# Kernel tuning notes

Measured on AMD Instinct MI355X. Metric: run time of the kernel, lower is better.

The kernel has to match this reference:

```python
import jax, jax.numpy as jnp
import numpy as np

N, D, H = 4096, 1024, 2048


def positional_encoding(d_model, n):
    even_i = jnp.arange(0, d_model, 2, dtype=jnp.float32)
    denom = jnp.power(jnp.float32(10000.0), even_i / d_model)
    pos = jnp.arange(n, dtype=jnp.float32)[:, None]            # (N,1)
    even_pe = jnp.sin(pos / denom)                             # (N,D/2)
    odd_pe = jnp.cos(pos / denom)                              # (N,D/2)
    # interleave sin/cos: stack on axis 2 then flatten -> (N, D)
    return jnp.stack([even_pe, odd_pe], axis=2).reshape(n, d_model)


def setup_inputs() -> dict:
    key = jax.random.key(0)
    ks = jax.random.split(key, 5)
    X = jax.random.normal(ks[0], (N, D), dtype=jnp.float32)
    mask = jnp.ones((N,), dtype=jnp.int32)  # unused by the module
    Wv = jax.random.normal(ks[1], (D, D), dtype=jnp.float32) * 0.02
    bv = jnp.zeros((D,), dtype=jnp.float32)
    W1 = jax.random.normal(ks[2], (2 * D, H), dtype=jnp.float32) * 0.02
    b1 = jnp.zeros((H,), dtype=jnp.float32)
    W2 = jax.random.normal(ks[3], (H, N), dtype=jnp.float32) * 0.02
    b2 = jnp.zeros((N,), dtype=jnp.float32)
    return {"X": X, "mask": mask, "Wv": Wv, "bv": bv,
            "W1": W1, "b1": b1, "W2": W2, "b2": b2}


def reference(X, mask, Wv, bv, W1, b1, W2, b2):
    n, d = X.shape
    V = X @ Wv + bv                                            # (N,D)
    PE = positional_encoding(d, n).astype(X.dtype)
    E = PE * X                                                 # (N,D)
    # leave-one-out mean: (global sum - row_i) / (N-1)  [replaces O(N^2) loop]
    loo = (jnp.sum(E, axis=0, keepdims=True) - E) / (n - 1)    # (N,D)
    feat = jnp.concatenate([X, loo], axis=1)                   # (N,2D)
    hidden = jax.nn.relu(feat @ W1 + b1)                       # (N,H)
    att_scores = hidden @ W2 + b2                              # (N,N)
    att_weights = jax.nn.softmax(att_scores, axis=-1)          # (N,N)
    # dropout p=0 (inference) -> identity
    return att_weights @ V                                     # (N,D)
```

## Files before the change

### kernel.cpp

```cpp
#include <hip/hip_runtime.h>
#include <hip/hip_bf16.h>

#define TOK 4096
#define DIM 1024
#define HID 2048
#define LN10K 9.210340371976184f

typedef __bf16 bh;
typedef __bf16 v8bf __attribute__((ext_vector_type(8)));
typedef float v4f __attribute__((ext_vector_type(4)));

typedef const __attribute__((address_space(1))) void* gvp;
typedef __attribute__((address_space(3))) void* svp;

__device__ __forceinline__ void gl_lds16(const bh* g, bh* s) {
  __builtin_amdgcn_global_load_lds((gvp)g, (svp)s, 16, 0, 0);
}

__global__ __launch_bounds__(256) void prep_x_colsum(const float* __restrict__ X,
                                                     bh* __restrict__ featb,
                                                     float* __restrict__ S) {
  int cp = blockIdx.x * 256 + threadIdx.x;
  int c = cp * 2;
  int r0 = blockIdx.y * 16;
  float inv_denom = __expf(-(float)c * (LN10K / (float)DIM));
  float s0 = 0.f, s1 = 0.f;
#pragma unroll 4
  for (int r = r0; r < r0 + 16; ++r) {
    float2 x = *(const float2*)(X + (size_t)r * DIM + c);
    float sn, cs;
    __sincosf((float)r * inv_denom, &sn, &cs);
    s0 += sn * x.x;
    s1 += cs * x.y;
    bh pair[2] = {(bh)x.x, (bh)x.y};
    *(ushort2*)(featb + (size_t)r * (2 * DIM) + c) = *(ushort2*)pair;
  }
  atomicAdd(&S[c], s0);
  atomicAdd(&S[c + 1], s1);
}

__global__ __launch_bounds__(256) void prep_loo(const float* __restrict__ X,
                                                const float* __restrict__ S,
                                                bh* __restrict__ featb) {
  size_t e4 = ((size_t)blockIdx.x * 256 + threadIdx.x) * 4;
  int r = (int)(e4 >> 10);
  int c = (int)(e4 & 1023);
  float4 x = *(const float4*)(X + e4);
  float4 s = *(const float4*)(S + c);
  float id0 = __expf(-(float)c * (LN10K / (float)DIM));
  float id1 = __expf(-(float)(c + 2) * (LN10K / (float)DIM));
  float sn0, cs0, sn1, cs1;
  __sincosf((float)r * id0, &sn0, &cs0);
  __sincosf((float)r * id1, &sn1, &cs1);
  const float inv = 1.0f / (float)(TOK - 1);
  bh outv[4];
  outv[0] = (bh)((s.x - sn0 * x.x) * inv);
  outv[1] = (bh)((s.y - cs0 * x.y) * inv);
  outv[2] = (bh)((s.z - sn1 * x.z) * inv);
  outv[3] = (bh)((s.w - cs1 * x.w) * inv);
  *(ushort4*)(featb + (size_t)r * (2 * DIM) + DIM + c) = *(ushort4*)outv;
}

__global__ __launch_bounds__(256) void transpose_all(const float* __restrict__ Wv,
                                                     const float* __restrict__ W1,
                                                     const float* __restrict__ W2,
                                                     bh* __restrict__ WvT,
                                                     bh* __restrict__ W1T,
                                                     bh* __restrict__ W2T) {
  __shared__ float tile[32][33];
  int bid = blockIdx.x;
  const float* in; bh* out; int Ncol, R, bx, by;
  if (bid < 1024)      { in = Wv; out = WvT; Ncol = DIM; R = DIM;
                         bx = bid & 31; by = bid >> 5; }
  else if (bid < 5120) { int b = bid - 1024; in = W1; out = W1T; Ncol = HID; R = 2 * DIM;
                         bx = b & 63; by = b >> 6; }
  else                 { int b = bid - 5120; in = W2; out = W2T; Ncol = TOK; R = HID;
                         bx = b & 127; by = b >> 7; }
  int nb = bx * 32, rb = by * 32;
  int tx = threadIdx.x, ty = threadIdx.y;
#pragma unroll
  for (int j = 0; j < 32; j += 8)
    tile[ty + j][tx] = in[(size_t)(rb + ty + j) * Ncol + nb + tx];
  __syncthreads();
#pragma unroll
  for (int j = 0; j < 32; j += 8)
    out[(size_t)(nb + ty + j) * R + rb + tx] = (bh)tile[tx][ty + j];
}

template <int BN, bool RELU, bool TROUT, bool EXPS, typename OutT>
__global__ __launch_bounds__(128, 2) void gemm_bt(const bh* __restrict__ A,
                                                  const bh* __restrict__ BT,
                                                  const float* __restrict__ bias,
                                                  OutT* __restrict__ C,
                                                  float* __restrict__ rowsum,
                                                  int K, int lda, int ldbt, int ldc) {
  constexpr int NT = BN / 16;
  __shared__ bh As[128 * 64];
  __shared__ bh Bs[BN * 64];
  const int t = threadIdx.x;
  const int id = blockIdx.x;
  const int bm = (id & 31) * 128, bn = (id >> 5) * BN;

  const int sr = t >> 3;
  const int c8 = ((t & 7) ^ (sr & 7)) * 8;
  const bh* gA = A + (size_t)(bm + sr) * lda + c8;
  const bh* gB = BT + (size_t)(bn + sr) * ldbt + c8;
  bh* sA = As + t * 8;
  bh* sB = Bs + t * 8;

  const int lane = t & 63, w = t >> 6;
  const int lc = lane & 15, q = lane >> 4;

  v4f acc[4][NT] = {};
  for (int k0 = 0; k0 < K; k0 += 64) {
#pragma unroll
    for (int j = 0; j < 8; ++j)
      gl_lds16(gA + k0 + j * 16 * lda, sA + j * 1024);
#pragma unroll
    for (int j = 0; j < NT; ++j)
      gl_lds16(gB + k0 + j * 16 * ldbt, sB + j * 1024);
    __syncthreads();
#pragma unroll
    for (int h = 0; h < 2; ++h) {
      const int off = ((h * 4 + q) ^ (lc & 7)) * 8;
      v8bf af[4], bfr[NT];
#pragma unroll
      for (int mt = 0; mt < 4; ++mt)
        af[mt] = *(const v8bf*)(As + (w * 64 + mt * 16 + lc) * 64 + off);
#pragma unroll
      for (int nt = 0; nt < NT; ++nt)
        bfr[nt] = *(const v8bf*)(Bs + (nt * 16 + lc) * 64 + off);
#pragma unroll
      for (int mt = 0; mt < 4; ++mt)
#pragma unroll
        for (int nt = 0; nt < NT; ++nt)
          acc[mt][nt] = __builtin_amdgcn_mfma_f32_16x16x32_bf16(af[mt], bfr[nt], acc[mt][nt], 0, 0, 0);
    }
    __syncthreads();
  }

  const int r4 = q * 4;
  if (EXPS) {
    float bbv[NT];
#pragma unroll
    for (int nt = 0; nt < NT; ++nt) bbv[nt] = bias ? bias[bn + nt * 16 + lc] : 0.0f;
#pragma unroll
    for (int mt = 0; mt < 4; ++mt) {
#pragma unroll
      for (int r = 0; r < 4; ++r) {
        int row = bm + w * 64 + mt * 16 + r4 + r;
        float rs = 0.0f;
#pragma unroll
        for (int nt = 0; nt < NT; ++nt) {
          float val = __expf(acc[mt][nt][r] + bbv[nt]);
          rs += val;
          C[(size_t)row * ldc + bn + nt * 16 + lc] = (OutT)val;
        }
        rs += __shfl_xor(rs, 1);
        rs += __shfl_xor(rs, 2);
        rs += __shfl_xor(rs, 4);
        rs += __shfl_xor(rs, 8);
        if (lc == 0) atomicAdd(rowsum + row, rs);
      }
    }
  } else {
#pragma unroll
    for (int mt = 0; mt < 4; ++mt) {
      int row0 = bm + w * 64 + mt * 16 + r4;
#pragma unroll
      for (int nt = 0; nt < NT; ++nt) {
        int col = bn + nt * 16 + lc;
        float bb = bias ? bias[col] : 0.0f;
#pragma unroll
        for (int r = 0; r < 4; ++r) {
          float val = acc[mt][nt][r] + bb;
          if (RELU) val = fmaxf(val, 0.0f);
          if (TROUT) C[(size_t)col * ldc + (row0 + r)] = (OutT)val;
          else       C[(size_t)(row0 + r) * ldc + col] = (OutT)val;
        }
      }
    }
  }
}

__global__ __launch_bounds__(256, 4) void gemm4_split(const bh* __restrict__ A,
                                                      const bh* __restrict__ BT,
                                                      float* __restrict__ C0,
                                                      float* __restrict__ C1) {
  __shared__ bh As[128 * 64];
  __shared__ bh Bs[128 * 64];
  const int t = threadIdx.x;
  const int id = blockIdx.x;
  const int bm = (id & 31) * 128, bn = (id >> 5) * 128;
  const int kbeg = blockIdx.y * (TOK / 2);

  const int sr = t >> 3;
  const int c8 = ((t & 7) ^ (sr & 7)) * 8;
  const bh* gA = A + (size_t)(bm + sr) * TOK + kbeg + c8;
  const bh* gB = BT + (size_t)(bn + sr) * TOK + kbeg + c8;
  bh* sA = As + t * 8;
  bh* sB = Bs + t * 8;

  const int lane = t & 63, w = t >> 6;
  const int wm = (w >> 1) * 64, wn = (w & 1) * 64;
  const int lc = lane & 15, q = lane >> 4;

  v4f acc[4][4] = {};
  for (int k0 = 0; k0 < TOK / 2; k0 += 64) {
#pragma unroll
    for (int j = 0; j < 4; ++j) {
      gl_lds16(gA + k0 + (size_t)(j * 32) * TOK, sA + j * 2048);
      gl_lds16(gB + k0 + (size_t)(j * 32) * TOK, sB + j * 2048);
    }
    __syncthreads();
#pragma unroll
    for (int h = 0; h < 2; ++h) {
      const int off = ((h * 4 + q) ^ (lc & 7)) * 8;
      v8bf af[4], bfr[4];
#pragma unroll
      for (int mt = 0; mt < 4; ++mt)
        af[mt] = *(const v8bf*)(As + (wm + mt * 16 + lc) * 64 + off);
#pragma unroll
      for (int nt = 0; nt < 4; ++nt)
        bfr[nt] = *(const v8bf*)(Bs + (wn + nt * 16 + lc) * 64 + off);
#pragma unroll
      for (int mt = 0; mt < 4; ++mt)
#pragma unroll
        for (int nt = 0; nt < 4; ++nt)
          acc[mt][nt] = __builtin_amdgcn_mfma_f32_16x16x32_bf16(af[mt], bfr[nt], acc[mt][nt], 0, 0, 0);
    }
    __syncthreads();
  }

  float* C = blockIdx.y ? C1 : C0;
  const int r4 = q * 4;
#pragma unroll
  for (int mt = 0; mt < 4; ++mt) {
    int row0 = bm + wm + mt * 16 + r4;
#pragma unroll
    for (int nt = 0; nt < 4; ++nt) {
      int col = bn + wn + nt * 16 + lc;
#pragma unroll
      for (int r = 0; r < 4; ++r)
        C[(size_t)(row0 + r) * DIM + col] = acc[mt][nt][r];
    }
  }
}

__global__ __launch_bounds__(256) void finalize(const float* __restrict__ p0,
                                                const float* __restrict__ p1,
                                                const float* __restrict__ rowsum,
                                                float* __restrict__ out) {
  size_t i = ((size_t)blockIdx.x * 256 + threadIdx.x) * 4;
  int row = (int)(i >> 10);
  float inv = 1.0f / rowsum[row];
  float4 a = *(const float4*)(p0 + i);
  float4 b = *(const float4*)(p1 + i);
  float4 o;
  o.x = (a.x + b.x) * inv; o.y = (a.y + b.y) * inv;
  o.z = (a.z + b.z) * inv; o.w = (a.w + b.w) * inv;
  *(float4*)(out + i) = o;
}

extern "C" void kernel_launch(void* const* d_in, const int* in_sizes, int n_in,
                              void* d_out, int out_size, void* d_ws, size_t ws_size,
                              hipStream_t stream) {
  (void)in_sizes; (void)n_in; (void)out_size; (void)ws_size;
  const float* X  = (const float*)d_in[0];
  const float* Wv = (const float*)d_in[2];
  const float* bv = (const float*)d_in[3];
  const float* W1 = (const float*)d_in[4];
  const float* b1 = (const float*)d_in[5];
  const float* W2 = (const float*)d_in[6];
  const float* b2 = (const float*)d_in[7];
  float* out = (float*)d_out;

  char* ws = (char*)d_ws;
  bh* featb = (bh*)(ws);
  bh* WvT   = (bh*)(ws + (16u << 20));
  bh* W1T   = (bh*)(ws + (18u << 20));
  bh* W2T   = (bh*)(ws + (26u << 20));
  bh* Vt    = (bh*)(ws + (42u << 20));
  bh* hid   = (bh*)(ws + (50u << 20));
  bh* scr   = (bh*)(ws + (66u << 20));
  float* S  = (float*)(ws + (98u << 20));
  float* rowsum = (float*)(ws + (98u << 20) + 4096);
  float* part0 = (float*)(ws);
  float* part1 = (float*)(ws + (26u << 20));

  hipError_t e = hipMemsetAsync(S, 0, 4096 + 4096 * sizeof(float), stream);
  (void)e;
  prep_x_colsum<<<dim3(DIM / 512, TOK / 16), 256, 0, stream>>>(X, featb, S);
  prep_loo<<<dim3((TOK * DIM) / 1024), 256, 0, stream>>>(X, S, featb);
  transpose_all<<<dim3(1024 + 4096 + 8192), dim3(32, 8), 0, stream>>>(
      Wv, W1, W2, WvT, W1T, W2T);

  gemm_bt<64, false, true, false, bh><<<dim3(32 * (DIM / 64)), 128, 0, stream>>>(
      featb, WvT, bv, Vt, nullptr, DIM, 2 * DIM, DIM, TOK);
  gemm_bt<128, true, false, false, bh><<<dim3(32 * (HID / 128)), 128, 0, stream>>>(
      featb, W1T, b1, hid, nullptr, 2 * DIM, 2 * DIM, 2 * DIM, HID);
  gemm_bt<128, false, false, true, bh><<<dim3(32 * (TOK / 128)), 128, 0, stream>>>(
      hid, W2T, b2, scr, rowsum, HID, HID, HID, TOK);
  gemm4_split<<<dim3(256, 2), 256, 0, stream>>>(scr, Vt, part0, part1);
  finalize<<<dim3((TOK * DIM) / 1024), 256, 0, stream>>>(part0, part1, rowsum, out);
}
```

Before: 322.2 us.

## Replace scores GEMM with 256x256-tile triple-buffered exp kernel

Adds a dedicated kernel for the hidden@W2 score GEMM that computes 256x256 output tiles with 8 waves of 512 threads. It stages operands into LDS through a three-buffer ring using direct global-to-LDS loads and interleaves staging with MFMA halves. The epilogue applies bias and exp, stores bf16 scores and atomically accumulates row sums. Larger tiles raise data reuse and cut global traffic, at the cost of more registers, only 256 blocks, and more barriers per K step.

```diff
diff --git a/kernel.cpp b/kernel.cpp
--- a/kernel.cpp
+++ b/kernel.cpp
@@ -183,6 +183,119 @@
   }
 }
 
+__global__ __launch_bounds__(512, 2) void gemm_exp256(const bh* __restrict__ A,
+                                                      const bh* __restrict__ BT,
+                                                      const float* __restrict__ bias,
+                                                      bh* __restrict__ C,
+                                                      float* __restrict__ rowsum) {
+  __shared__ bh As[3 * 8192];
+  __shared__ bh Bs[3 * 8192];
+  const int t = threadIdx.x;
+  const int id = blockIdx.x;
+  const int bm = (id & 15) * 256, bn = (id >> 4) * 256;
+  const int lane = t & 63, w = t >> 6;
+  const int wm = (w >> 2) * 128, wn = (w & 3) * 64;
+  const int lc = lane & 15, q = lane >> 4;
+  const int csw = (q ^ ((lc >> 1) & 3)) * 8;
+
+  const int srow = t >> 2;
+  const int sc = (t & 3) ^ ((t >> 3) & 3);
+  const bh* gA = A + (size_t)(bm + srow) * HID + sc * 8;
+  const bh* gB = BT + (size_t)(bn + srow) * HID + sc * 8;
+  bh* sA = As + t * 8;
+  bh* sB = Bs + t * 8;
+
+  auto stage_a = [&](int kt, int buf) {
+    const bh* g = gA + (size_t)kt * 32;
+    bh* s = sA + buf * 8192;
+    gl_lds16(g, s);
+    gl_lds16(g + (size_t)128 * HID, s + 4096);
+  };
+  auto stage_b = [&](int kt, int buf) {
+    const bh* g = gB + (size_t)kt * 32;
+    bh* s = sB + buf * 8192;
+    gl_lds16(g, s);
+    gl_lds16(g + (size_t)128 * HID, s + 4096);
+  };
+
+  v4f acc[8][4] = {};
+
+  stage_a(0, 0); stage_b(0, 0);
+  stage_a(1, 1); stage_b(1, 1);
+  asm volatile("s_waitcnt vmcnt(4)" ::: "memory");
+  __builtin_amdgcn_s_barrier();
+  __builtin_amdgcn_sched_barrier(0);
+
+  int cur = 0, nxt = 2;
+  for (int kt = 0; kt < 64; ++kt) {
+    const bh* ab = As + cur * 8192;
+    const bh* bb = Bs + cur * 8192;
+    v8bf af[4], bf[4];
+#pragma unroll
+    for (int mt = 0; mt < 4; ++mt)
+      af[mt] = *(const v8bf*)(ab + (wm + mt * 16 + lc) * 32 + csw);
+#pragma unroll
+    for (int nt = 0; nt < 4; ++nt)
+      bf[nt] = *(const v8bf*)(bb + (wn + nt * 16 + lc) * 32 + csw);
+    if (kt < 62) stage_a(kt + 2, nxt);
+    __builtin_amdgcn_s_barrier();
+    __builtin_amdgcn_sched_barrier(0);
+    __builtin_amdgcn_s_setprio(1);
+#pragma unroll
+    for (int mt = 0; mt < 4; ++mt)
+#pragma unroll
+      for (int nt = 0; nt < 4; ++nt)
+        acc[mt][nt] = __builtin_amdgcn_mfma_f32_16x16x32_bf16(af[mt], bf[nt], acc[mt][nt], 0, 0, 0);
+    __builtin_amdgcn_s_setprio(0);
+    __builtin_amdgcn_s_barrier();
+    __builtin_amdgcn_sched_barrier(0);
+    v8bf ah[4];
+#pragma unroll
+    for (int mt = 0; mt < 4; ++mt)
+      ah[mt] = *(const v8bf*)(ab + (wm + 64 + mt * 16 + lc) * 32 + csw);
+    if (kt < 62) stage_b(kt + 2, nxt);
+    __builtin_amdgcn_s_barrier();
+    __builtin_amdgcn_sched_barrier(0);
+    __builtin_amdgcn_s_setprio(1);
+#pragma unroll
+    for (int mt = 0; mt < 4; ++mt)
+#pragma unroll
+      for (int nt = 0; nt < 4; ++nt)
+        acc[4 + mt][nt] = __builtin_amdgcn_mfma_f32_16x16x32_bf16(ah[mt], bf[nt], acc[4 + mt][nt], 0, 0, 0);
+    __builtin_amdgcn_s_setprio(0);
+    if (kt < 62)       asm volatile("s_waitcnt vmcnt(4)" ::: "memory");
+    else if (kt == 62) asm volatile("s_waitcnt vmcnt(0)" ::: "memory");
+    __builtin_amdgcn_s_barrier();
+    __builtin_amdgcn_sched_barrier(0);
+    cur = (cur == 2) ? 0 : cur + 1;
+    nxt = (nxt == 2) ? 0 : nxt + 1;
+  }
+
+  const int r4 = q * 4;
+  float bbv[4];
+#pragma unroll
+  for (int nt = 0; nt < 4; ++nt) bbv[nt] = bias[bn + wn + nt * 16 + lc];
+#pragma unroll
+  for (int mt = 0; mt < 8; ++mt) {
+#pragma unroll
+    for (int r = 0; r < 4; ++r) {
+      int row = bm + wm + mt * 16 + r4 + r;
+      float rs = 0.0f;
+#pragma unroll
+      for (int nt = 0; nt < 4; ++nt) {
+        float val = __expf(acc[mt][nt][r] + bbv[nt]);
+        rs += val;
+        C[(size_t)row * TOK + bn + wn + nt * 16 + lc] = (bh)val;
+      }
+      rs += __shfl_xor(rs, 1);
+      rs += __shfl_xor(rs, 2);
+      rs += __shfl_xor(rs, 4);
+      rs += __shfl_xor(rs, 8);
+      if (lc == 0) atomicAdd(rowsum + row, rs);
+    }
+  }
+}
+
 __global__ __launch_bounds__(256, 4) void gemm4_split(const bh* __restrict__ A,
                                                       const bh* __restrict__ BT,
                                                       float* __restrict__ C0,
@@ -299,8 +412,7 @@
       featb, WvT, bv, Vt, nullptr, DIM, 2 * DIM, DIM, TOK);
   gemm_bt<128, true, false, false, bh><<<dim3(32 * (HID / 128)), 128, 0, stream>>>(
       featb, W1T, b1, hid, nullptr, 2 * DIM, 2 * DIM, 2 * DIM, HID);
-  gemm_bt<128, false, false, true, bh><<<dim3(32 * (TOK / 128)), 128, 0, stream>>>(
-      hid, W2T, b2, scr, rowsum, HID, HID, HID, TOK);
+  gemm_exp256<<<dim3(256), 512, 0, stream>>>(hid, W2T, b2, scr, rowsum);
   gemm4_split<<<dim3(256, 2), 256, 0, stream>>>(scr, Vt, part0, part1);
   finalize<<<dim3((TOK * DIM) / 1024), 256, 0, stream>>>(part0, part1, rowsum, out);
 }
```

New measurement: 330.6 us. 1.03x slower.

## Add 256x256 tiled exp GEMM with 4-stage LDS pipeline for attention scores

Applied to the files above, without the earlier changes.

Replaces the generic 128-tile GEMM that computes the exp'd attention scores with a specialised kernel. It uses 512 threads per block, 256x256 output tiles and a 4-slot LDS ring filled by direct global-to-LDS loads. Prefetch runs two tiles ahead with explicit vmcnt waits and raised priority around the MFMA block. The goal is more operand reuse per byte loaded and better overlap of loads with MFMA on the largest GEMM. In exchange it needs more LDS and registers per block, so occupancy is lower, and fewer blocks (256) fill the chip.

```diff
diff --git a/kernel.cpp b/kernel.cpp
--- a/kernel.cpp
+++ b/kernel.cpp
@@ -183,6 +183,110 @@
   }
 }
 
+__global__ __launch_bounds__(512, 2) void gemm_exp256(const bh* __restrict__ A,
+                                                      const bh* __restrict__ BT,
+                                                      const float* __restrict__ bias,
+                                                      bh* __restrict__ C,
+                                                      float* __restrict__ rowsum) {
+  __shared__ bh As[4 * 8192];
+  __shared__ bh Bs[4 * 8192];
+  const int t = threadIdx.x;
+  const int id = blockIdx.x;
+  const int bm = (id & 15) * 256, bn = (id >> 4) * 256;
+  const int lane = t & 63, w = t >> 6;
+  const int wm = (w >> 2) * 128, wn = (w & 3) * 64;
+  const int lc = lane & 15, q = lane >> 4;
+  const int csw = (q ^ ((lc >> 1) & 3)) * 8;
+
+  const int srow = t >> 2;
+  const int sc = (t & 3) ^ ((t >> 3) & 3);
+  const bh* gA = A + (size_t)(bm + srow) * HID + sc * 8;
+  const bh* gB = BT + (size_t)(bn + srow) * HID + sc * 8;
+  bh* sA = As + t * 8;
+  bh* sB = Bs + t * 8;
+
+  v4f acc[8][4] = {};
+
+#define STAGE(kt, slot)                                                        \
+  do {                                                                         \
+    gl_lds16(gA + (kt) * 32, sA + (slot) * 8192);                              \
+    gl_lds16(gA + (kt) * 32 + (size_t)128 * HID, sA + (slot) * 8192 + 4096);   \
+    gl_lds16(gB + (kt) * 32, sB + (slot) * 8192);                              \
+    gl_lds16(gB + (kt) * 32 + (size_t)128 * HID, sB + (slot) * 8192 + 4096);   \
+  } while (0)
+
+#define TILE(kt, slot, STG, WMODE)                                             \
+  do {                                                                         \
+    const bh* ab = As + (slot) * 8192;                                         \
+    const bh* bb = Bs + (slot) * 8192;                                         \
+    v8bf af[4], ah[4], bfr[4];                                                 \
+    _Pragma("unroll") for (int mt = 0; mt < 4; ++mt)                           \
+        af[mt] = *(const v8bf*)(ab + (wm + mt * 16 + lc) * 32 + csw);          \
+    _Pragma("unroll") for (int nt = 0; nt < 4; ++nt)                           \
+        bfr[nt] = *(const v8bf*)(bb + (wn + nt * 16 + lc) * 32 + csw);         \
+    _Pragma("unroll") for (int mt = 0; mt < 4; ++mt)                           \
+        ah[mt] = *(const v8bf*)(ab + (wm + 64 + mt * 16 + lc) * 32 + csw);     \
+    if (STG) STAGE((kt) + 2, ((slot) + 2) & 3);                                \
+    __builtin_amdgcn_s_setprio(1);                                             \
+    _Pragma("unroll") for (int mt = 0; mt < 4; ++mt)                           \
+        _Pragma("unroll") for (int nt = 0; nt < 4; ++nt)                       \
+            acc[mt][nt] = __builtin_amdgcn_mfma_f32_16x16x32_bf16(             \
+                af[mt], bfr[nt], acc[mt][nt], 0, 0, 0);                        \
+    _Pragma("unroll") for (int mt = 0; mt < 4; ++mt)                           \
+        _Pragma("unroll") for (int nt = 0; nt < 4; ++nt)                       \
+            acc[4 + mt][nt] = __builtin_amdgcn_mfma_f32_16x16x32_bf16(         \
+                ah[mt], bfr[nt], acc[4 + mt][nt], 0, 0, 0);                    \
+    __builtin_amdgcn_s_setprio(0);                                             \
+    if ((WMODE) == 1) asm volatile("s_waitcnt vmcnt(4)" ::: "memory");         \
+    if ((WMODE) == 2) asm volatile("s_waitcnt vmcnt(0)" ::: "memory");         \
+    if ((WMODE) != 0) __builtin_amdgcn_s_barrier();                            \
+  } while (0)
+
+  STAGE(0, 0);
+  STAGE(1, 1);
+  asm volatile("s_waitcnt vmcnt(4)" ::: "memory");
+  __builtin_amdgcn_s_barrier();
+
+  for (int ko = 0; ko < 15; ++ko) {
+    const int kb = ko * 4;
+    TILE(kb + 0, 0, true, 1);
+    TILE(kb + 1, 1, true, 1);
+    TILE(kb + 2, 2, true, 1);
+    TILE(kb + 3, 3, true, 1);
+  }
+  TILE(60, 0, true, 1);
+  TILE(61, 1, true, 1);
+  TILE(62, 2, false, 2);
+  TILE(63, 3, false, 0);
+
+#undef TILE
+#undef STAGE
+
+  const int r4 = q * 4;
+  float bbv[4];
+#pragma unroll
+  for (int nt = 0; nt < 4; ++nt) bbv[nt] = bias[bn + wn + nt * 16 + lc];
+#pragma unroll
+  for (int mt = 0; mt < 8; ++mt) {
+#pragma unroll
+    for (int r = 0; r < 4; ++r) {
+      int row = bm + wm + mt * 16 + r4 + r;
+      float rs = 0.0f;
+#pragma unroll
+      for (int nt = 0; nt < 4; ++nt) {
+        float val = __expf(acc[mt][nt][r] + bbv[nt]);
+        rs += val;
+        C[(size_t)row * TOK + bn + wn + nt * 16 + lc] = (bh)val;
+      }
+      rs += __shfl_xor(rs, 1);
+      rs += __shfl_xor(rs, 2);
+      rs += __shfl_xor(rs, 4);
+      rs += __shfl_xor(rs, 8);
+      if (lc == 0) atomicAdd(rowsum + row, rs);
+    }
+  }
+}
+
 __global__ __launch_bounds__(256, 4) void gemm4_split(const bh* __restrict__ A,
                                                       const bh* __restrict__ BT,
                                                       float* __restrict__ C0,
@@ -299,8 +403,7 @@
       featb, WvT, bv, Vt, nullptr, DIM, 2 * DIM, DIM, TOK);
   gemm_bt<128, true, false, false, bh><<<dim3(32 * (HID / 128)), 128, 0, stream>>>(
       featb, W1T, b1, hid, nullptr, 2 * DIM, 2 * DIM, 2 * DIM, HID);
-  gemm_bt<128, false, false, true, bh><<<dim3(32 * (TOK / 128)), 128, 0, stream>>>(
-      hid, W2T, b2, scr, rowsum, HID, HID, HID, TOK);
+  gemm_exp256<<<dim3(256), 512, 0, stream>>>(hid, W2T, b2, scr, rowsum);
   gemm4_split<<<dim3(256, 2), 256, 0, stream>>>(scr, Vt, part0, part1);
   finalize<<<dim3((TOK * DIM) / 1024), 256, 0, stream>>>(part0, part1, rowsum, out);
 }
```

Result: no change. 328.2 us (+1.9%).

## Replace scores GEMM with 256x256-tile pipelined exp kernel

Applied to the files above, without the earlier changes.

Adds a dedicated kernel for the hidden@W2 scores GEMM that uses 256x256 block tiles, 8 waves, and double-buffered direct global-to-LDS loads. The loads for later k-tiles are interleaved between quarter-tile MFMA phases, with barriers and raised wave priority around each phase. The exp epilogue and row-sum atomics are fused in as before. The aim is higher operand reuse and better overlap of memory traffic with MFMA on the largest GEMM. The cost is more LDS and registers per block, and hand-tuned waitcnt counts that must match the issued loads exactly.

```diff
diff --git a/kernel.cpp b/kernel.cpp
--- a/kernel.cpp
+++ b/kernel.cpp
@@ -183,6 +183,151 @@
   }
 }
 
+__global__ __launch_bounds__(512, 2) void gemm_exp256(const bh* __restrict__ A,
+                                                      const bh* __restrict__ BT,
+                                                      const float* __restrict__ bias,
+                                                      bh* __restrict__ C,
+                                                      float* __restrict__ rowsum) {
+  __shared__ bh As[2][16384];
+  __shared__ bh Bs[2][16384];
+  const int t = threadIdx.x;
+  const int id = blockIdx.x;
+  const int bm = (id & 15) * 256, bn = (id >> 4) * 256;
+  const int lane = t & 63, w = t >> 6;
+  const int wm = (w >> 2) * 128, wn = (w & 3) * 64;
+  const int lc = lane & 15, q = lane >> 4;
+  const int e0 = q ^ (lc & 7);
+
+  const int srow = t >> 3;
+  const int schunk = (t & 7) ^ (srow & 7);
+  const bh* gA = A + (size_t)(bm + srow) * HID + schunk * 8;
+  const bh* gB = BT + (size_t)(bn + srow) * HID + schunk * 8;
+  bh* sA = &As[0][0] + t * 8;
+  bh* sB = &Bs[0][0] + t * 8;
+
+  v4f acc[8][4] = {};
+
+#define STG_A(kt, c, buf) \
+  gl_lds16(gA + (size_t)(kt) * 64 + (size_t)((c) * 64) * HID, sA + (buf) * 16384 + (c) * 4096)
+#define STG_B(kt, c, buf) \
+  gl_lds16(gB + (size_t)(kt) * 64 + (size_t)((c) * 64) * HID, sB + (buf) * 16384 + (c) * 4096)
+
+#define TILE64(kt, buf, STG1, STG23, WM)                                        \
+  do {                                                                          \
+    const bh* ab = &As[buf][0];                                                 \
+    const bh* bb = &Bs[buf][0];                                                 \
+    v8bf alo[4][2], ahi[4][2], blo[2][2], bhi2[2][2];                           \
+                                                             \
+    _Pragma("unroll") for (int mt = 0; mt < 4; ++mt)                            \
+      _Pragma("unroll") for (int kk = 0; kk < 2; ++kk)                          \
+        alo[mt][kk] = *(const v8bf*)(ab + (wm + mt * 16 + lc) * 64 +            \
+                                     ((e0 ^ (kk << 2)) << 3));                  \
+    _Pragma("unroll") for (int nt = 0; nt < 2; ++nt)                            \
+      _Pragma("unroll") for (int kk = 0; kk < 2; ++kk)                          \
+        blo[nt][kk] = *(const v8bf*)(bb + (wn + nt * 16 + lc) * 64 +            \
+                                     ((e0 ^ (kk << 2)) << 3));                  \
+    if (STG1) { STG_B((kt) + 1, 2, (buf) ^ 1); STG_B((kt) + 1, 3, (buf) ^ 1); } \
+    __builtin_amdgcn_s_barrier();                                               \
+    asm volatile("s_waitcnt lgkmcnt(0)" ::: "memory");                          \
+    __builtin_amdgcn_s_setprio(1);                                              \
+    _Pragma("unroll") for (int mt = 0; mt < 4; ++mt)                            \
+      _Pragma("unroll") for (int nt = 0; nt < 2; ++nt)                          \
+        _Pragma("unroll") for (int kk = 0; kk < 2; ++kk)                        \
+          acc[mt][nt] = __builtin_amdgcn_mfma_f32_16x16x32_bf16(                \
+              alo[mt][kk], blo[nt][kk], acc[mt][nt], 0, 0, 0);                  \
+    __builtin_amdgcn_s_setprio(0);                                              \
+    __builtin_amdgcn_s_barrier();                                               \
+                                                             \
+    _Pragma("unroll") for (int nt = 0; nt < 2; ++nt)                            \
+      _Pragma("unroll") for (int kk = 0; kk < 2; ++kk)                          \
+        bhi2[nt][kk] = *(const v8bf*)(bb + (wn + 32 + nt * 16 + lc) * 64 +      \
+                                      ((e0 ^ (kk << 2)) << 3));                 \
+    if (STG23) { STG_A((kt) + 2, 0, buf); STG_A((kt) + 2, 2, buf); }            \
+    __builtin_amdgcn_s_barrier();                                               \
+    asm volatile("s_waitcnt lgkmcnt(0)" ::: "memory");                          \
+    __builtin_amdgcn_s_setprio(1);                                              \
+    _Pragma("unroll") for (int mt = 0; mt < 4; ++mt)                            \
+      _Pragma("unroll") for (int nt = 0; nt < 2; ++nt)                          \
+        _Pragma("unroll") for (int kk = 0; kk < 2; ++kk)                        \
+          acc[mt][2 + nt] = __builtin_amdgcn_mfma_f32_16x16x32_bf16(            \
+              alo[mt][kk], bhi2[nt][kk], acc[mt][2 + nt], 0, 0, 0);             \
+    __builtin_amdgcn_s_setprio(0);                                              \
+    __builtin_amdgcn_s_barrier();                                               \
+                                                             \
+    _Pragma("unroll") for (int mt = 0; mt < 4; ++mt)                            \
+      _Pragma("unroll") for (int kk = 0; kk < 2; ++kk)                          \
+        ahi[mt][kk] = *(const v8bf*)(ab + (wm + 64 + mt * 16 + lc) * 64 +       \
+                                     ((e0 ^ (kk << 2)) << 3));                  \
+    if (STG23) { STG_B((kt) + 2, 0, buf); STG_B((kt) + 2, 1, buf); }            \
+    __builtin_amdgcn_s_barrier();                                               \
+    asm volatile("s_waitcnt lgkmcnt(0)" ::: "memory");                          \
+    __builtin_amdgcn_s_setprio(1);                                              \
+    _Pragma("unroll") for (int mt = 0; mt < 4; ++mt)                            \
+      _Pragma("unroll") for (int nt = 0; nt < 2; ++nt)                          \
+        _Pragma("unroll") for (int kk = 0; kk < 2; ++kk)                        \
+          acc[4 + mt][nt] = __builtin_amdgcn_mfma_f32_16x16x32_bf16(            \
+              ahi[mt][kk], blo[nt][kk], acc[4 + mt][nt], 0, 0, 0);              \
+    __builtin_amdgcn_s_setprio(0);                                              \
+    __builtin_amdgcn_s_barrier();                                               \
+                                                             \
+    if (STG23) { STG_A((kt) + 2, 1, buf); STG_A((kt) + 2, 3, buf); }            \
+    __builtin_amdgcn_s_barrier();                                               \
+    __builtin_amdgcn_s_setprio(1);                                              \
+    _Pragma("unroll") for (int mt = 0; mt < 4; ++mt)                            \
+      _Pragma("unroll") for (int nt = 0; nt < 2; ++nt)                          \
+        _Pragma("unroll") for (int kk = 0; kk < 2; ++kk)                        \
+          acc[4 + mt][2 + nt] = __builtin_amdgcn_mfma_f32_16x16x32_bf16(        \
+              ahi[mt][kk], bhi2[nt][kk], acc[4 + mt][2 + nt], 0, 0, 0);         \
+    __builtin_amdgcn_s_setprio(0);                                              \
+    if ((WM) == 1) asm volatile("s_waitcnt vmcnt(6)" ::: "memory");             \
+    if ((WM) == 2) asm volatile("s_waitcnt vmcnt(0)" ::: "memory");             \
+    __builtin_amdgcn_s_barrier();                                               \
+  } while (0)
+
+  STG_A(0, 0, 0); STG_A(0, 1, 0); STG_A(0, 2, 0); STG_A(0, 3, 0);
+  STG_B(0, 0, 0); STG_B(0, 1, 0); STG_B(0, 2, 0); STG_B(0, 3, 0);
+  STG_A(1, 0, 1); STG_A(1, 2, 1); STG_B(1, 0, 1); STG_B(1, 1, 1);
+  STG_A(1, 1, 1); STG_A(1, 3, 1);
+  asm volatile("s_waitcnt vmcnt(6)" ::: "memory");
+  __builtin_amdgcn_s_barrier();
+
+  for (int tp = 0; tp < 15; ++tp) {
+    const int kt = tp * 2;
+    TILE64(kt, 0, 1, 1, 1);
+    TILE64(kt + 1, 1, 1, 1, 1);
+  }
+  TILE64(30, 0, 1, 0, 2);
+  TILE64(31, 1, 0, 0, 0);
+
+#undef TILE64
+#undef STG_A
+#undef STG_B
+
+  const int r4 = q * 4;
+  float bbv[4];
+#pragma unroll
+  for (int nt = 0; nt < 4; ++nt) bbv[nt] = bias[bn + wn + nt * 16 + lc];
+#pragma unroll
+  for (int mt = 0; mt < 8; ++mt) {
+#pragma unroll
+    for (int r = 0; r < 4; ++r) {
+      int row = bm + wm + mt * 16 + r4 + r;
+      float rs = 0.0f;
+#pragma unroll
+      for (int nt = 0; nt < 4; ++nt) {
+        float val = __expf(acc[mt][nt][r] + bbv[nt]);
+        rs += val;
+        C[(size_t)row * TOK + bn + wn + nt * 16 + lc] = (bh)val;
+      }
+      rs += __shfl_xor(rs, 1);
+      rs += __shfl_xor(rs, 2);
+      rs += __shfl_xor(rs, 4);
+      rs += __shfl_xor(rs, 8);
+      if (lc == 0) atomicAdd(rowsum + row, rs);
+    }
+  }
+}
+
 __global__ __launch_bounds__(256, 4) void gemm4_split(const bh* __restrict__ A,
                                                       const bh* __restrict__ BT,
                                                       float* __restrict__ C0,
@@ -299,8 +444,7 @@
       featb, WvT, bv, Vt, nullptr, DIM, 2 * DIM, DIM, TOK);
   gemm_bt<128, true, false, false, bh><<<dim3(32 * (HID / 128)), 128, 0, stream>>>(
       featb, W1T, b1, hid, nullptr, 2 * DIM, 2 * DIM, 2 * DIM, HID);
-  gemm_bt<128, false, false, true, bh><<<dim3(32 * (TOK / 128)), 128, 0, stream>>>(
-      hid, W2T, b2, scr, rowsum, HID, HID, HID, TOK);
+  gemm_exp256<<<dim3(256), 512, 0, stream>>>(hid, W2T, b2, scr, rowsum);
   gemm4_split<<<dim3(256, 2), 256, 0, stream>>>(scr, Vt, part0, part1);
   finalize<<<dim3((TOK * DIM) / 1024), 256, 0, stream>>>(part0, part1, rowsum, out);
 }
```

Measured after the change: 327.5 us. About the same (+1.6%).
